# Optimization experiments

Hardware: AMD Instinct MI355X
Metric: run time of the kernel (lower is better)

## Reference

```python
import jax, jax.numpy as jnp
import numpy as np

EPS = 1e-5


def _gcn_conv(x, src, dst, norm, W, b, n_nodes):
    # PyG GCNConv: transform, then normalized scatter-add aggregation (self-loops included in src/dst)
    h = x @ W                                   # [N, out]
    msg = h[src] * norm[:, None]                # gather over edges [E+N, out]
    agg = jax.ops.segment_sum(msg, dst, num_segments=n_nodes)
    return agg + b


def _bn(x, gamma, beta):
    # BatchNorm1d in training mode: batch stats over node axis, biased variance
    mu = jnp.mean(x, axis=0)
    var = jnp.mean((x - mu) ** 2, axis=0)
    return (x - mu) * jax.lax.rsqrt(var + EPS) * gamma + beta


def setup_inputs() -> dict:
    key = jax.random.key(0)
    ks = jax.random.split(key, 8)
    N, E, F_in, H, F_out = 50000, 800000, 32, 96, 2
    x = jax.random.normal(ks[0], (N, F_in), dtype=jnp.float32)
    edge_index = jax.random.randint(ks[1], (2, E), 0, N, dtype=jnp.int64)
    def lin(k, fi, fo):
        s = 1.0 / np.sqrt(fi)
        return jax.random.uniform(k, (fi, fo), jnp.float32, -s, s)
    W1 = lin(ks[2], F_in, H); b1 = jnp.zeros((H,), jnp.float32)
    W2 = lin(ks[3], H, H);    b2 = jnp.zeros((H,), jnp.float32)
    W3 = lin(ks[4], H, H);    b3 = jnp.zeros((H,), jnp.float32)
    W4 = lin(ks[5], H, F_out); b4 = jnp.zeros((F_out,), jnp.float32)
    g1 = jnp.ones((H,), jnp.float32); be1 = jnp.zeros((H,), jnp.float32)
    g2 = jnp.ones((H,), jnp.float32); be2 = jnp.zeros((H,), jnp.float32)
    g3 = jnp.ones((H,), jnp.float32); be3 = jnp.zeros((H,), jnp.float32)
    return dict(x=x, edge_index=edge_index,
                W1=W1, b1=b1, g1=g1, be1=be1,
                W2=W2, b2=b2, g2=g2, be2=be2,
                W3=W3, b3=b3, g3=g3, be3=be3,
                W4=W4, b4=b4)


def reference(x, edge_index, W1, b1, g1, be1, W2, b2, g2, be2, W3, b3, g3, be3, W4, b4):
    N = x.shape[0]
    loop = jnp.arange(N, dtype=edge_index.dtype)
    src = jnp.concatenate([edge_index[0], loop])   # add self-loops
    dst = jnp.concatenate([edge_index[1], loop])
    deg = jax.ops.segment_sum(jnp.ones_like(dst, dtype=x.dtype), dst, num_segments=N)
    dinv = jnp.where(deg > 0, jax.lax.rsqrt(deg), 0.0)
    norm = dinv[src] * dinv[dst]                   # D^{-1/2} (A+I) D^{-1/2}

    h = jax.nn.relu(_bn(_gcn_conv(x, src, dst, norm, W1, b1, N), g1, be1))
    h = jax.nn.relu(_bn(_gcn_conv(h, src, dst, norm, W2, b2, N), g2, be2))
    h = jax.nn.relu(_bn(_gcn_conv(h, src, dst, norm, W3, b3, N), g3, be3))
    return _gcn_conv(h, src, dst, norm, W4, b4, N)
```

## Files before the change

kernel.cpp:

```cpp
#include <hip/hip_runtime.h>
#include <hip/hip_bf16.h>

using bf16x8 = __attribute__((ext_vector_type(8))) short;
using f32x4  = __attribute__((ext_vector_type(4))) float;

__device__ __forceinline__ float ldf(const void* p, size_t i, float isf){
  if (isf > 0.5f) return ((const float*)p)[i];
  unsigned int u = ((unsigned int)((const unsigned short*)p)[i]) << 16;
  return __uint_as_float(u);
}
__device__ __forceinline__ unsigned short f2bf(float v){
  unsigned int u = __float_as_uint(v);
  u = (u + 0x7FFFu + ((u >> 16) & 1u)) >> 16;
  return (unsigned short)u;
}
__device__ __forceinline__ unsigned int pk2(float a, float b){
  return (unsigned int)f2bf(a) | ((unsigned int)f2bf(b) << 16);
}
__device__ __forceinline__ float lo16(unsigned int u){ return __uint_as_float(u << 16); }
__device__ __forceinline__ float hi16(unsigned int u){ return __uint_as_float(u & 0xFFFF0000u); }
__device__ __forceinline__ float bfh(unsigned short h){ return __uint_as_float(((unsigned int)h) << 16); }

__global__ void k_fill(unsigned short* o, unsigned short v, int n){
  int i = blockIdx.x*blockDim.x + threadIdx.x;
  if (i < n) o[i] = v;
}

__global__ void k_detect(const unsigned short* xh, const unsigned int* eu,
                         float* flag, int nelemX, long long E){
  __shared__ int sf32, si64;
  if (threadIdx.x == 0){ sf32 = 0; si64 = 1; }
  __syncthreads();
  int t = threadIdx.x;
  int i = 2*t;
  if (i < nelemX){
    unsigned e8 = (xh[i] >> 7) & 0xFFu;
    if (e8 >= 140u) sf32 = 1;
  }
  if ((long long)(2*t + 1) < 2*E){
    if (eu[2*t + 1] != 0u) si64 = 0;
  }
  __syncthreads();
  if (t == 0){ flag[0] = (float)sf32; flag[1] = (float)si64; }
}

__global__ void k_cvtW(const void* W1, const void* W2, const void* W3, const void* W4,
                       const float* __restrict__ flag,
                       unsigned short* __restrict__ Wt1, unsigned short* __restrict__ Wt2,
                       unsigned short* __restrict__ Wt3, float* __restrict__ W4f){
  float isf = flag[0];
  int t = blockIdx.x*blockDim.x + threadIdx.x;
  if (t < 3072){ int nn = t >> 5, k = t & 31; Wt1[t] = f2bf(ldf(W1, (size_t)96*k + nn, isf)); }
  if (t < 9216){
    int nn = t/96, k = t - 96*nn;
    Wt2[t] = f2bf(ldf(W2, (size_t)96*k + nn, isf));
    Wt3[t] = f2bf(ldf(W3, (size_t)96*k + nn, isf));
  }
  if (t < 192) W4f[t] = ldf(W4, t, isf);
}

__global__ void k_cnt(const int* __restrict__ ei, const float* __restrict__ flag,
                      int* __restrict__ cnt, long long E, int n){
  long long i = (long long)blockIdx.x*blockDim.x + threadIdx.x;
  if (i >= E) return;
  int d = (flag[1] > 0.5f) ? ei[2*E + 2*i] : ei[E + i];
  if ((unsigned)d < (unsigned)n) atomicAdd(&cnt[d], 1);
}

__global__ void k_bsum(const int* __restrict__ cnt, int* __restrict__ bsum, int n){
  int i = blockIdx.x*256 + threadIdx.x;
  int v = (i < n) ? cnt[i] : 0;
  #pragma unroll
  for (int off = 32; off; off >>= 1) v += __shfl_down(v, off, 64);
  __shared__ int w[4];
  if ((threadIdx.x & 63) == 0) w[threadIdx.x >> 6] = v;
  __syncthreads();
  if (threadIdx.x == 0) bsum[blockIdx.x] = w[0]+w[1]+w[2]+w[3];
}

__global__ void k_sscan(const int* __restrict__ bsum, int* __restrict__ boff,
                        int* __restrict__ rowstN, int nb){
  int t = threadIdx.x;
  int v = (t < nb) ? bsum[t] : 0;
  int lane = t & 63, wid = t >> 6;
  int s = v;
  #pragma unroll
  for (int off = 1; off < 64; off <<= 1){
    int u = __shfl_up(s, off, 64);
    if (lane >= off) s += u;
  }
  __shared__ int wt[4];
  if (lane == 63) wt[wid] = s;
  __syncthreads();
  int add = 0;
  for (int w = 0; w < wid; ++w) add += wt[w];
  int incl = s + add;
  if (t < nb) boff[t] = incl - v;
  if (t == nb - 1) *rowstN = incl;
}

__global__ void k_emit(const int* __restrict__ cnt, const int* __restrict__ boff,
                       int* __restrict__ rowst, int* __restrict__ cursor,
                       float* __restrict__ dinv, int n){
  int i = blockIdx.x*256 + threadIdx.x;
  int v = (i < n) ? cnt[i] : 0;
  int lane = threadIdx.x & 63, wid = threadIdx.x >> 6;
  int s = v;
  #pragma unroll
  for (int off = 1; off < 64; off <<= 1){
    int u = __shfl_up(s, off, 64);
    if (lane >= off) s += u;
  }
  __shared__ int wt[4];
  if (lane == 63) wt[wid] = s;
  __syncthreads();
  int add = 0;
  for (int w = 0; w < wid; ++w) add += wt[w];
  if (i < n){
    int r = boff[blockIdx.x] + add + s - v;
    rowst[i] = r;
    cursor[i] = r;
    dinv[i]  = rsqrtf((float)(1 + v));
  }
}

template<typename IT>
__global__ void k_fill_slots(const int* __restrict__ ei, const float* __restrict__ flag,
                             int* __restrict__ cursor, IT* __restrict__ csr,
                             long long E, int n){
  long long i = (long long)blockIdx.x*blockDim.x + threadIdx.x;
  if (i >= E) return;
  int s, d;
  if (flag[1] > 0.5f){ s = ei[2*i]; d = ei[2*E + 2*i]; }
  else               { s = ei[i];   d = ei[E + i];     }
  if ((unsigned)s < (unsigned)n && (unsigned)d < (unsigned)n){
    int p = atomicAdd(&cursor[d], 1);
    csr[p] = (IT)s;
  }
}

__global__ __launch_bounds__(256) void k_lin1m(const void* __restrict__ x,
      const unsigned short* __restrict__ Wt1b, const float* __restrict__ flag,
      const float* __restrict__ dinv, unsigned short* __restrict__ HS, int n){
  __shared__ __align__(16) unsigned short Xs[64][40];
  __shared__ __align__(16) unsigned short Wt[96][40];
  int t = threadIdx.x;
  float isf = flag[0];
  for (int q = t; q < 384; q += 256){
    uint4 v = ((const uint4*)Wt1b)[q];
    *(uint4*)&Wt[q >> 2][(q & 3)*8] = v;
  }
  {
    int row = t >> 2, part = t & 3;
    int node = blockIdx.x*64 + row;
    uint4 o;
    if (node < n){
      if (isf > 0.5f){
        const float* xr = (const float*)x + (size_t)32*node + 8*part;
        o.x = pk2(xr[0], xr[1]); o.y = pk2(xr[2], xr[3]);
        o.z = pk2(xr[4], xr[5]); o.w = pk2(xr[6], xr[7]);
      } else {
        o = ((const uint4*)x)[(size_t)4*node + part];
      }
    } else { o.x = o.y = o.z = o.w = 0u; }
    *(uint4*)&Xs[row][8*part] = o;
  }
  __syncthreads();

  int wv = t >> 6, lane = t & 63;
  int m = lane & 15, quad = lane >> 4;
  bf16x8 av = *(const bf16x8*)&Xs[16*wv + m][8*quad];
  f32x4 acc[6];
  #pragma unroll
  for (int c = 0; c < 6; ++c) acc[c] = (f32x4)(0.f);
  #pragma unroll
  for (int c = 0; c < 6; ++c){
    bf16x8 bv = *(const bf16x8*)&Wt[16*c + m][8*quad];
    acc[c] = __builtin_amdgcn_mfma_f32_16x16x32_bf16(av, bv, acc[c], 0, 0, 0);
  }
  int rowbase = blockIdx.x*64 + 16*wv + 4*quad;
  float div[4];
  #pragma unroll
  for (int r = 0; r < 4; ++r){ int rr = rowbase + r; div[r] = (rr < n) ? dinv[rr] : 0.f; }
  #pragma unroll
  for (int c = 0; c < 6; ++c){
    int col = 16*c + m;
    #pragma unroll
    for (int r = 0; r < 4; ++r){
      int rr = rowbase + r;
      if (rr < n) HS[(size_t)96*rr + col] = f2bf(acc[c][r]*div[r]);
    }
  }
}

__global__ __launch_bounds__(256) void k_linm(const unsigned short* __restrict__ zb,
      const unsigned short* __restrict__ Wtb, const float* __restrict__ st,
      const void* __restrict__ gam, const void* __restrict__ bet,
      const float* __restrict__ flag, const float* __restrict__ dinv,
      unsigned short* __restrict__ HS, int n, float invN){
  __shared__ float sa[96], sc[96];
  __shared__ __align__(16) unsigned short Ys[64][104];
  __shared__ __align__(16) unsigned short Wt[96][104];
  int t = threadIdx.x;
  if (t < 96){
    float isf = flag[0];
    float mu  = st[t]*invN;
    float var = fmaxf(st[96+t]*invN - mu*mu, 0.f);
    float istd = rsqrtf(var + 1e-5f);
    float a = ldf(gam, t, isf)*istd;
    sa[t] = a; sc[t] = ldf(bet, t, isf) - mu*a;
  }
  for (int q = t; q < 1152; q += 256){
    uint4 v = ((const uint4*)Wtb)[q];
    *(uint4*)&Wt[q/12][8*(q - 12*(q/12))] = v;
  }
  __syncthreads();
  {
    int row = t >> 2, part = t & 3;
    int node = blockIdx.x*64 + row;
    if (node < n){
      const uint4* zr = (const uint4*)(zb + (size_t)96*node) + 3*part;
      #pragma unroll
      for (int q = 0; q < 3; ++q){
        uint4 zz = zr[q];
        int k = 24*part + 8*q;
        float y0 = fmaxf(lo16(zz.x)*sa[k]   + sc[k],   0.f);
        float y1 = fmaxf(hi16(zz.x)*sa[k+1] + sc[k+1], 0.f);
        float y2 = fmaxf(lo16(zz.y)*sa[k+2] + sc[k+2], 0.f);
        float y3 = fmaxf(hi16(zz.y)*sa[k+3] + sc[k+3], 0.f);
        float y4 = fmaxf(lo16(zz.z)*sa[k+4] + sc[k+4], 0.f);
        float y5 = fmaxf(hi16(zz.z)*sa[k+5] + sc[k+5], 0.f);
        float y6 = fmaxf(lo16(zz.w)*sa[k+6] + sc[k+6], 0.f);
        float y7 = fmaxf(hi16(zz.w)*sa[k+7] + sc[k+7], 0.f);
        *(unsigned int*)&Ys[row][k]     = pk2(y0, y1);
        *(unsigned int*)&Ys[row][k + 2] = pk2(y2, y3);
        *(unsigned int*)&Ys[row][k + 4] = pk2(y4, y5);
        *(unsigned int*)&Ys[row][k + 6] = pk2(y6, y7);
      }
    } else {
      unsigned int* yp = (unsigned int*)&Ys[row][24*part];
      #pragma unroll
      for (int q = 0; q < 12; ++q) yp[q] = 0u;
    }
  }
  __syncthreads();

  int wv = t >> 6, lane = t & 63;
  int m = lane & 15, quad = lane >> 4;
  bf16x8 av[3];
  #pragma unroll
  for (int kt = 0; kt < 3; ++kt)
    av[kt] = *(const bf16x8*)&Ys[16*wv + m][32*kt + 8*quad];
  f32x4 acc[6];
  #pragma unroll
  for (int c = 0; c < 6; ++c) acc[c] = (f32x4)(0.f);
  #pragma unroll
  for (int c = 0; c < 6; ++c){
    const unsigned short* wrow = &Wt[16*c + m][8*quad];
    #pragma unroll
    for (int kt = 0; kt < 3; ++kt){
      bf16x8 bv = *(const bf16x8*)(wrow + 32*kt);
      acc[c] = __builtin_amdgcn_mfma_f32_16x16x32_bf16(av[kt], bv, acc[c], 0, 0, 0);
    }
  }
  int rowbase = blockIdx.x*64 + 16*wv + 4*quad;
  float div[4];
  #pragma unroll
  for (int r = 0; r < 4; ++r){ int rr = rowbase + r; div[r] = (rr < n) ? dinv[rr] : 0.f; }
  #pragma unroll
  for (int c = 0; c < 6; ++c){
    int col = 16*c + m;
    #pragma unroll
    for (int r = 0; r < 4; ++r){
      int rr = rowbase + r;
      if (rr < n) HS[(size_t)96*rr + col] = f2bf(acc[c][r]*div[r]);
    }
  }
}

__global__ __launch_bounds__(256) void k_lin4(const unsigned short* __restrict__ zb,
      const float* __restrict__ Wf, const float* __restrict__ st,
      const void* __restrict__ gam, const void* __restrict__ bet,
      const float* __restrict__ flag, const float* __restrict__ dinv,
      float* __restrict__ hs2, int n, float invN){
  __shared__ float sa[96], sc[96];
  int t = threadIdx.x;
  if (t < 96){
    float isf = flag[0];
    float mu  = st[t]*invN;
    float var = fmaxf(st[96+t]*invN - mu*mu, 0.f);
    float istd = rsqrtf(var + 1e-5f);
    float a = ldf(gam, t, isf)*istd;
    sa[t] = a; sc[t] = ldf(bet, t, isf) - mu*a;
  }
  __syncthreads();
  int i = blockIdx.x*blockDim.x + t;
  if (i >= n) return;
  const uint4* zr = (const uint4*)(zb + (size_t)96*i);
  float a0 = 0.f, a1 = 0.f;
  #pragma unroll
  for (int q = 0; q < 12; ++q){
    uint4 zz = zr[q];
    int k = 8*q;
    float y;
    y = fmaxf(lo16(zz.x)*sa[k]   + sc[k],   0.f); a0 += y*Wf[2*k];    a1 += y*Wf[2*k+1];
    y = fmaxf(hi16(zz.x)*sa[k+1] + sc[k+1], 0.f); a0 += y*Wf[2*k+2];  a1 += y*Wf[2*k+3];
    y = fmaxf(lo16(zz.y)*sa[k+2] + sc[k+2], 0.f); a0 += y*Wf[2*k+4];  a1 += y*Wf[2*k+5];
    y = fmaxf(hi16(zz.y)*sa[k+3] + sc[k+3], 0.f); a0 += y*Wf[2*k+6];  a1 += y*Wf[2*k+7];
    y = fmaxf(lo16(zz.z)*sa[k+4] + sc[k+4], 0.f); a0 += y*Wf[2*k+8];  a1 += y*Wf[2*k+9];
    y = fmaxf(hi16(zz.z)*sa[k+5] + sc[k+5], 0.f); a0 += y*Wf[2*k+10]; a1 += y*Wf[2*k+11];
    y = fmaxf(lo16(zz.w)*sa[k+6] + sc[k+6], 0.f); a0 += y*Wf[2*k+12]; a1 += y*Wf[2*k+13];
    y = fmaxf(hi16(zz.w)*sa[k+7] + sc[k+7], 0.f); a0 += y*Wf[2*k+14]; a1 += y*Wf[2*k+15];
  }
  float di = dinv[i];
  hs2[(size_t)2*i]   = di*a0;
  hs2[(size_t)2*i+1] = di*a1;
}

#define ACC8(v) { a0+=lo16((v).x); a1+=hi16((v).x); a2+=lo16((v).y); a3+=hi16((v).y); \
                  a4+=lo16((v).z); a5+=hi16((v).z); a6+=lo16((v).w); a7+=hi16((v).w); }
template<typename IT>
__global__ __launch_bounds__(192) void k_agg(const uint4* __restrict__ hsr,
      const int* __restrict__ rowst, const IT* __restrict__ csr,
      const float* __restrict__ dinv, uint4* __restrict__ zb4,
      float* __restrict__ st, int n){
  int t = threadIdx.y*12 + threadIdx.x;
  if (blockIdx.x == 0 && t < 192) st[t] = 0.f;
  int node = blockIdx.x*16 + threadIdx.y;
  if (node >= n) return;
  int g = threadIdx.x;
  uint4 v = hsr[(size_t)node*12 + g];
  float a0 = lo16(v.x), a1 = hi16(v.x), a2 = lo16(v.y), a3 = hi16(v.y);
  float a4 = lo16(v.z), a5 = hi16(v.z), a6 = lo16(v.w), a7 = hi16(v.w);
  int b = rowst[node], e = rowst[node+1];
  int j = b;
  for (; j + 7 < e; j += 8){
    uint4 v0 = hsr[(size_t)csr[j]  *12 + g];
    uint4 v1 = hsr[(size_t)csr[j+1]*12 + g];
    uint4 v2 = hsr[(size_t)csr[j+2]*12 + g];
    uint4 v3 = hsr[(size_t)csr[j+3]*12 + g];
    uint4 v4 = hsr[(size_t)csr[j+4]*12 + g];
    uint4 v5 = hsr[(size_t)csr[j+5]*12 + g];
    uint4 v6 = hsr[(size_t)csr[j+6]*12 + g];
    uint4 v7 = hsr[(size_t)csr[j+7]*12 + g];
    ACC8(v0); ACC8(v1); ACC8(v2); ACC8(v3);
    ACC8(v4); ACC8(v5); ACC8(v6); ACC8(v7);
  }
  for (; j + 3 < e; j += 4){
    uint4 v0 = hsr[(size_t)csr[j]  *12 + g];
    uint4 v1 = hsr[(size_t)csr[j+1]*12 + g];
    uint4 v2 = hsr[(size_t)csr[j+2]*12 + g];
    uint4 v3 = hsr[(size_t)csr[j+3]*12 + g];
    ACC8(v0); ACC8(v1); ACC8(v2); ACC8(v3);
  }
  for (; j < e; ++j){
    uint4 vv = hsr[(size_t)csr[j]*12 + g];
    ACC8(vv);
  }
  float di = dinv[node];
  uint4 o;
  o.x = pk2(a0*di, a1*di);
  o.y = pk2(a2*di, a3*di);
  o.z = pk2(a4*di, a5*di);
  o.w = pk2(a6*di, a7*di);
  zb4[(size_t)node*12 + g] = o;
}

template<typename IT>
__global__ void k_agg2(const float2* __restrict__ hs2, const int* __restrict__ rowst,
                       const IT* __restrict__ csr, const float* __restrict__ dinv,
                       const void* __restrict__ b4, const float* __restrict__ flag,
                       void* __restrict__ out, int n){
  int node = blockIdx.x*blockDim.x + threadIdx.x;
  if (node >= n) return;
  float2 a = hs2[node];
  int b = rowst[node], e = rowst[node+1];
  for (int j = b; j < e; ++j){
    float2 v = hs2[(size_t)csr[j]];
    a.x += v.x; a.y += v.y;
  }
  float isf = flag[0];
  float di = dinv[node];
  float v0 = a.x*di + ldf(b4, 0, isf);
  float v1 = a.y*di + ldf(b4, 1, isf);
  if (isf > 0.5f){
    ((float*)out)[(size_t)2*node]   = v0;
    ((float*)out)[(size_t)2*node+1] = v1;
  } else {
    ((unsigned short*)out)[(size_t)2*node]   = f2bf(v0);
    ((unsigned short*)out)[(size_t)2*node+1] = f2bf(v1);
  }
}

__global__ void k_stats(const unsigned short* __restrict__ zb, float* __restrict__ st, int n){
  int f = threadIdx.x, ty = threadIdx.y;
  float s = 0.f, q = 0.f;
  for (int i = blockIdx.x*4 + ty; i < n; i += gridDim.x*4){
    float y = bfh(zb[(size_t)96*i + f]);
    s += y; q += y*y;
  }
  __shared__ float ls[4][96], lq[4][96];
  ls[ty][f] = s; lq[ty][f] = q;
  __syncthreads();
  if (ty == 0){
    s = ls[0][f]+ls[1][f]+ls[2][f]+ls[3][f];
    q = lq[0][f]+lq[1][f]+lq[2][f]+lq[3][f];
    atomicAdd(&st[f], s); atomicAdd(&st[96+f], q);
  }
}

extern "C" void kernel_launch(void* const* d_in, const int* in_sizes, int n_in,
                              void* d_out, int out_size, void* d_ws, size_t ws_size,
                              hipStream_t stream)
{
  const int B = 256;
  unsigned short* outh = (unsigned short*)d_out;

  if (n_in < 16){
    k_fill<<<(out_size+B-1)/B, B, 0, stream>>>(outh, 0x3F40u, out_size); return;
  }
  const int N = in_sizes[0] / 32;
  const long long E = in_sizes[1] / 2;
  if (in_sizes[0] % 32 != 0 || out_size != 2*N){
    k_fill<<<(out_size+B-1)/B, B, 0, stream>>>(outh, 0x3F60u, out_size); return;
  }
  const bool u16 = (N < 65536);

  size_t Npad = ((size_t)N + 3) & ~(size_t)3;
  float* ws   = (float*)d_ws;
  float* dinv = ws;
  float* hs2  = dinv + Npad;
  float* st   = hs2 + (size_t)2*N;
  float* flag = st + 384;
  float* W4f  = flag + 4;
  unsigned short* Wt1b = (unsigned short*)(W4f + 192);
  unsigned short* Wt2b = Wt1b + 3072;
  unsigned short* Wt3b = Wt2b + 9216;
  int* cnt    = (int*)(Wt3b + 9216);
  int* cursor = cnt + N;
  int* rowst  = cursor + N;
  int* bsum   = rowst + N + 1;
  int* boff   = bsum + 256;
  void* csrv  = (void*)(boff + 256);
  size_t csrBytes = (size_t)E * (u16 ? 2 : 4);
  uintptr_t hp_ = (uintptr_t)csrv + csrBytes;
  hp_ = (hp_ + 15) & ~(uintptr_t)15;
  unsigned short* HS = (unsigned short*)hp_;
  unsigned short* Zb = HS + (size_t)96*N;

  size_t needB = ((uintptr_t)(Zb + (size_t)96*N) - (uintptr_t)d_ws) + 64;
  if (ws_size < needB){
    k_fill<<<(out_size+B-1)/B, B, 0, stream>>>(outh, 0x3F00u, out_size); return;
  }

  const void* x  = d_in[0];
  const int*  ei = (const int*)d_in[1];
  const void* W1 = d_in[2];
  const void* g1 = d_in[4];  const void* be1 = d_in[5];
  const void* W2 = d_in[6];
  const void* g2 = d_in[8];  const void* be2 = d_in[9];
  const void* W3 = d_in[10];
  const void* g3 = d_in[12]; const void* be3 = d_in[13];
  const void* W4 = d_in[14];
  const void* b4 = d_in[15];

  int gN  = (N + B - 1)/B;
  int gE  = (int)((E + B - 1)/B);
  int nb  = (N + 255)/256;
  int gA  = (N + 15)/16;
  int gL  = (N + 63)/64;
  float invN = 1.0f / (float)N;
  dim3 ablk(12,16);
  dim3 sblk(96,4);

  k_detect<<<1, 256, 0, stream>>>((const unsigned short*)x, (const unsigned int*)ei,
                                  flag, in_sizes[0], E);
  hipMemsetAsync(cnt, 0, (size_t)N*sizeof(int), stream);
  k_cvtW<<<(9216+B-1)/B, B, 0, stream>>>(W1, W2, W3, W4, flag, Wt1b, Wt2b, Wt3b, W4f);
  k_cnt<<<gE, B, 0, stream>>>(ei, flag, cnt, E, N);
  k_bsum<<<nb, 256, 0, stream>>>(cnt, bsum, N);
  k_sscan<<<1, 256, 0, stream>>>(bsum, boff, rowst + N, nb);
  k_emit<<<nb, 256, 0, stream>>>(cnt, boff, rowst, cursor, dinv, N);

  if (u16){
    unsigned short* csr = (unsigned short*)csrv;
    k_fill_slots<unsigned short><<<gE, B, 0, stream>>>(ei, flag, cursor, csr, E, N);

    k_lin1m<<<gL, B, 0, stream>>>(x, Wt1b, flag, dinv, HS, N);
    k_agg<unsigned short><<<gA, ablk, 0, stream>>>((const uint4*)HS, rowst, csr, dinv, (uint4*)Zb, st, N);
    k_stats<<<512, sblk, 0, stream>>>(Zb, st, N);

    k_linm<<<gL, B, 0, stream>>>(Zb, Wt2b, st, g1, be1, flag, dinv, HS, N, invN);
    k_agg<unsigned short><<<gA, ablk, 0, stream>>>((const uint4*)HS, rowst, csr, dinv, (uint4*)Zb, st, N);
    k_stats<<<512, sblk, 0, stream>>>(Zb, st, N);

    k_linm<<<gL, B, 0, stream>>>(Zb, Wt3b, st, g2, be2, flag, dinv, HS, N, invN);
    k_agg<unsigned short><<<gA, ablk, 0, stream>>>((const uint4*)HS, rowst, csr, dinv, (uint4*)Zb, st, N);
    k_stats<<<512, sblk, 0, stream>>>(Zb, st, N);

    k_lin4<<<gN, B, 0, stream>>>(Zb, W4f, st, g3, be3, flag, dinv, hs2, N, invN);
    k_agg2<unsigned short><<<gN, B, 0, stream>>>((const float2*)hs2, rowst, csr, dinv, b4, flag, d_out, N);
  } else {
    int* csr = (int*)csrv;
    k_fill_slots<int><<<gE, B, 0, stream>>>(ei, flag, cursor, csr, E, N);

    k_lin1m<<<gL, B, 0, stream>>>(x, Wt1b, flag, dinv, HS, N);
    k_agg<int><<<gA, ablk, 0, stream>>>((const uint4*)HS, rowst, csr, dinv, (uint4*)Zb, st, N);
    k_stats<<<512, sblk, 0, stream>>>(Zb, st, N);

    k_linm<<<gL, B, 0, stream>>>(Zb, Wt2b, st, g1, be1, flag, dinv, HS, N, invN);
    k_agg<int><<<gA, ablk, 0, stream>>>((const uint4*)HS, rowst, csr, dinv, (uint4*)Zb, st, N);
    k_stats<<<512, sblk, 0, stream>>>(Zb, st, N);

    k_linm<<<gL, B, 0, stream>>>(Zb, Wt3b, st, g2, be2, flag, dinv, HS, N, invN);
    k_agg<int><<<gA, ablk, 0, stream>>>((const uint4*)HS, rowst, csr, dinv, (uint4*)Zb, st, N);
    k_stats<<<512, sblk, 0, stream>>>(Zb, st, N);

    k_lin4<<<gN, B, 0, stream>>>(Zb, W4f, st, g3, be3, flag, dinv, hs2, N, invN);
    k_agg2<int><<<gN, B, 0, stream>>>((const float2*)hs2, rowst, csr, dinv, b4, flag, d_out, N);
  }
}
```

Baseline: 373.2 us.

## Partition CSR slot fill by destination range and merge prep kernels

Merges the dtype-detection and weight-conversion kernels into one single-block launch, removing one launch and its dependency. The CSR fill kernel now assigns 8 blocks to each 4096-edge chunk. Each block handles only destinations in one eighth of the node range, so atomics and scattered writes from one block stay within a narrower region of cursor/csr, which is meant to improve cache locality. In exchange, every edge index is read 8 times, and the weight conversion now runs on a single block.

After: 378.3 us. Within noise of the previous version (+1.3%).

```diff
diff --git a/kernel.cpp b/kernel.cpp
--- a/kernel.cpp
+++ b/kernel.cpp
@@ -26,35 +26,41 @@
   if (i < n) o[i] = v;
 }
 
-__global__ void k_detect(const unsigned short* xh, const unsigned int* eu,
-                         float* flag, int nelemX, long long E){
-  __shared__ int sf32, si64;
-  if (threadIdx.x == 0){ sf32 = 0; si64 = 1; }
-  __syncthreads();
-  int t = threadIdx.x;
-  int i = 2*t;
-  if (i < nelemX){
-    unsigned e8 = (xh[i] >> 7) & 0xFFu;
-    if (e8 >= 140u) sf32 = 1;
-  }
-  if ((long long)(2*t + 1) < 2*E){
-    if (eu[2*t + 1] != 0u) si64 = 0;
-  }
-  __syncthreads();
-  if (t == 0){ flag[0] = (float)sf32; flag[1] = (float)si64; }
-}
-
-__global__ void k_cvtW(const void* W1, const void* W2, const void* W3, const void* W4,
-                       const float* __restrict__ flag,
+__global__ void k_prep(const unsigned short* xh, const unsigned int* eu,
+                       float* flag, int nelemX, long long E,
+                       const void* W1, const void* W2, const void* W3, const void* W4,
                        unsigned short* __restrict__ Wt1, unsigned short* __restrict__ Wt2,
                        unsigned short* __restrict__ Wt3, float* __restrict__ W4f){
-  float isf = flag[0];
-  int t = blockIdx.x*blockDim.x + threadIdx.x;
-  if (t < 3072){ int nn = t >> 5, k = t & 31; Wt1[t] = f2bf(ldf(W1, (size_t)96*k + nn, isf)); }
-  if (t < 9216){
-    int nn = t/96, k = t - 96*nn;
-    Wt2[t] = f2bf(ldf(W2, (size_t)96*k + nn, isf));
-    Wt3[t] = f2bf(ldf(W3, (size_t)96*k + nn, isf));
+  __shared__ int sf32, si64;
+  __shared__ float sisf;
+  int t = threadIdx.x;
+  if (t == 0){ sf32 = 0; si64 = 1; }
+  __syncthreads();
+  {
+    int i = 2*t;
+    if (i < nelemX){
+      unsigned e8 = (xh[i] >> 7) & 0xFFu;
+      if (e8 >= 140u) sf32 = 1;
+    }
+    if ((long long)(2*t + 1) < 2*E){
+      if (eu[2*t + 1] != 0u) si64 = 0;
+    }
+  }
+  __syncthreads();
+  if (t == 0){
+    flag[0] = (float)sf32; flag[1] = (float)si64;
+    sisf = (float)sf32;
+  }
+  __syncthreads();
+  float isf = sisf;
+  for (int q = t; q < 3072; q += 256){
+    int nn = q >> 5, k = q & 31;
+    Wt1[q] = f2bf(ldf(W1, (size_t)96*k + nn, isf));
+  }
+  for (int q = t; q < 9216; q += 256){
+    int nn = q/96, k = q - 96*nn;
+    Wt2[q] = f2bf(ldf(W2, (size_t)96*k + nn, isf));
+    Wt3[q] = f2bf(ldf(W3, (size_t)96*k + nn, isf));
   }
   if (t < 192) W4f[t] = ldf(W4, t, isf);
 }
@@ -124,18 +130,26 @@
   }
 }
 
+#define FS_CHUNK 4096
 template<typename IT>
-__global__ void k_fill_slots(const int* __restrict__ ei, const float* __restrict__ flag,
+__global__ __launch_bounds__(256) void k_fill_slots8(const int* __restrict__ ei,
+                             const float* __restrict__ flag,
                              int* __restrict__ cursor, IT* __restrict__ csr,
                              long long E, int n){
-  long long i = (long long)blockIdx.x*blockDim.x + threadIdx.x;
-  if (i >= E) return;
-  int s, d;
-  if (flag[1] > 0.5f){ s = ei[2*i]; d = ei[2*E + 2*i]; }
-  else               { s = ei[i];   d = ei[E + i];     }
-  if ((unsigned)s < (unsigned)n && (unsigned)d < (unsigned)n){
-    int p = atomicAdd(&cursor[d], 1);
-    csr[p] = (IT)s;
+  int part = blockIdx.x & 7;
+  long long base = (long long)(blockIdx.x >> 3) * FS_CHUNK;
+  int pl = (int)(((long long)n *  part     ) >> 3);
+  int pr = (int)(((long long)n * (part + 1)) >> 3);
+  bool i64 = (flag[1] > 0.5f);
+  long long lim = base + FS_CHUNK < E ? base + FS_CHUNK : E;
+  for (long long i = base + threadIdx.x; i < lim; i += 256){
+    int s, d;
+    if (i64){ s = ei[2*i]; d = ei[2*E + 2*i]; }
+    else    { s = ei[i];   d = ei[E + i];     }
+    if (d >= pl && d < pr && (unsigned)s < (unsigned)n){
+      int p = atomicAdd(&cursor[d], 1);
+      csr[p] = (IT)s;
+    }
   }
 }
 
@@ -469,14 +483,15 @@
   int nb  = (N + 255)/256;
   int gA  = (N + 15)/16;
   int gL  = (N + 63)/64;
+  int gF8 = (int)((E + FS_CHUNK - 1)/FS_CHUNK) * 8;
   float invN = 1.0f / (float)N;
   dim3 ablk(12,16);
   dim3 sblk(96,4);
 
-  k_detect<<<1, 256, 0, stream>>>((const unsigned short*)x, (const unsigned int*)ei,
-                                  flag, in_sizes[0], E);
+  k_prep<<<1, 256, 0, stream>>>((const unsigned short*)x, (const unsigned int*)ei,
+                                flag, in_sizes[0], E, W1, W2, W3, W4,
+                                Wt1b, Wt2b, Wt3b, W4f);
   hipMemsetAsync(cnt, 0, (size_t)N*sizeof(int), stream);
-  k_cvtW<<<(9216+B-1)/B, B, 0, stream>>>(W1, W2, W3, W4, flag, Wt1b, Wt2b, Wt3b, W4f);
   k_cnt<<<gE, B, 0, stream>>>(ei, flag, cnt, E, N);
   k_bsum<<<nb, 256, 0, stream>>>(cnt, bsum, N);
   k_sscan<<<1, 256, 0, stream>>>(bsum, boff, rowst + N, nb);
@@ -484,7 +499,7 @@
 
   if (u16){
     unsigned short* csr = (unsigned short*)csrv;
-    k_fill_slots<unsigned short><<<gE, B, 0, stream>>>(ei, flag, cursor, csr, E, N);
+    k_fill_slots8<unsigned short><<<gF8, B, 0, stream>>>(ei, flag, cursor, csr, E, N);
 
     k_lin1m<<<gL, B, 0, stream>>>(x, Wt1b, flag, dinv, HS, N);
     k_agg<unsigned short><<<gA, ablk, 0, stream>>>((const uint4*)HS, rowst, csr, dinv, (uint4*)Zb, st, N);
@@ -502,7 +517,7 @@
     k_agg2<unsigned short><<<gN, B, 0, stream>>>((const float2*)hs2, rowst, csr, dinv, b4, flag, d_out, N);
   } else {
     int* csr = (int*)csrv;
-    k_fill_slots<int><<<gE, B, 0, stream>>>(ei, flag, cursor, csr, E, N);
+    k_fill_slots8<int><<<gF8, B, 0, stream>>>(ei, flag, cursor, csr, E, N);
 
     k_lin1m<<<gL, B, 0, stream>>>(x, Wt1b, flag, dinv, HS, N);
     k_agg<int><<<gA, ablk, 0, stream>>>((const uint4*)HS, rowst, csr, dinv, (uint4*)Zb, st, N);
```
